# Optimization experiments

Measured on AMD Instinct MI355X. Metric: run time of the kernel, lower is better.

The kernel has to match this reference:

```python
import jax, jax.numpy as jnp
import numpy as np

N, D, M = 4096, 2048, 1000
NL = 2048
MAX_ITER = 5


def setup_inputs() -> dict:
    key = jax.random.key(0)
    k1, k2, k3 = jax.random.split(key, 3)
    fc7 = jax.random.normal(k1, (N, D), dtype=jnp.float32)
    # prior probs: softmax over random logits (row-stochastic, like CNN softmax output)
    probs = jax.nn.softmax(jax.random.normal(k2, (N, M), dtype=jnp.float32), axis=-1)
    labs = jax.random.randint(k3, (NL,), 0, M)
    L = jnp.arange(NL)
    U = jnp.arange(NL, N)
    return {"fc7": fc7, "probs": probs, "labs": labs, "L": L, "U": U}


def _get_W_correlation(fc7):
    # Pearson correlation between rows, negatives clipped to zero (set_negative='hard')
    x = fc7 - fc7.mean(axis=1, keepdims=True)
    norms = jnp.linalg.norm(x, axis=1)  # [n]
    W = (x @ x.T) / jnp.outer(norms, norms)  # [n, n]
    return jax.nn.relu(W)


def _init_probs_prior(probs, labs, L, U):
    n, m = probs.shape
    ps = jnp.zeros((n, m), dtype=probs.dtype)
    ps = ps.at[U].set(probs[U])       # unlabeled: CNN prior
    ps = ps.at[L, labs].set(1.0)      # labeled: one-hot
    return ps


def _replicator(W, ps, max_iter):
    def step(p, _):
        q = p * (W @ p)                              # [n, m]
        q = q / jnp.sum(q, axis=1, keepdims=True)
        return q, None
    ps, _ = jax.lax.scan(step, ps, None, length=max_iter)
    return ps


def reference(fc7, probs, labs, L, U):
    W = _get_W_correlation(fc7)
    ps = _init_probs_prior(probs, labs, L, U)
    ps = _replicator(W, ps, MAX_ITER)
    return ps, W
```

## Files before the change

kernel.cpp:

```cpp
#include <hip/hip_runtime.h>
#include <stdint.h>

#define NS 4096
#define DD 2048
#define MC 1000
#define MP 1024
#define NLAB 2048
#define NU 2048

typedef __attribute__((ext_vector_type(8))) short bf16x8;
typedef __attribute__((ext_vector_type(4))) float f32x4;

__device__ inline unsigned short f2bf(float f) {
  union { float f; uint32_t u; } v; v.f = f;
  uint32_t u = v.u;
  u = u + 0x7fffu + ((u >> 16) & 1u);
  return (unsigned short)(u >> 16);
}
__device__ inline float bf2f(unsigned short h) {
  union { uint32_t u; float f; } v; v.u = ((uint32_t)h) << 16;
  return v.f;
}

__device__ inline void gload_lds16(const void* g, void* l) {
  __builtin_amdgcn_global_load_lds(
      (const __attribute__((address_space(1))) void*)g,
      (__attribute__((address_space(3))) void*)l, 16, 0, 0);
}

__device__ inline float block_sum(float v, float* sm, int tid) {
  #pragma unroll
  for (int o = 32; o > 0; o >>= 1) v += __shfl_down(v, o, 64);
  __syncthreads();
  if ((tid & 63) == 0) sm[tid >> 6] = v;
  __syncthreads();
  return sm[0] + sm[1] + sm[2] + sm[3];
}

__global__ void center_norm_k(const float* __restrict__ fc7,
                              unsigned short* __restrict__ Xc,
                              float* __restrict__ invn) {
  __shared__ float sm[4];
  const int row = blockIdx.x;
  const int tid = threadIdx.x;
  const float4* src = (const float4*)(fc7 + (size_t)row * DD);
  float4 a = src[tid * 2];
  float4 b = src[tid * 2 + 1];
  float s = a.x + a.y + a.z + a.w + b.x + b.y + b.z + b.w;
  s = block_sum(s, sm, tid);
  const float mean = s * (1.f / (float)DD);
  float v0 = a.x - mean, v1 = a.y - mean, v2 = a.z - mean, v3 = a.w - mean;
  float v4 = b.x - mean, v5 = b.y - mean, v6 = b.z - mean, v7 = b.w - mean;
  float ss = v0*v0 + v1*v1 + v2*v2 + v3*v3 + v4*v4 + v5*v5 + v6*v6 + v7*v7;
  ss = block_sum(ss, sm, tid);
  if (tid == 0) invn[row] = rsqrtf(ss);
  ushort4 o0 = make_ushort4(f2bf(v0), f2bf(v1), f2bf(v2), f2bf(v3));
  ushort4 o1 = make_ushort4(f2bf(v4), f2bf(v5), f2bf(v6), f2bf(v7));
  ushort4* dst = (ushort4*)(Xc + (size_t)row * DD);
  dst[tid * 2] = o0;
  dst[tid * 2 + 1] = o1;
}

__global__ void gemm_w_sym(const unsigned short* __restrict__ A,
                           const float* __restrict__ invn,
                           float* __restrict__ outF,
                           unsigned short* __restrict__ outBF) {
  __shared__ __align__(16) unsigned short As[64 * 64];
  __shared__ __align__(16) unsigned short Bs[128 * 64];
  const int tid = threadIdx.x;
  const int wv = tid >> 6;
  const int ln = tid & 63;
  const int wr = wv >> 1, wc = wv & 1;

  int b = (blockIdx.x & 7) * 132 + (blockIdx.x >> 3);
  int r = 0;
  while (b >= 32 - (r >> 1)) { b -= 32 - (r >> 1); ++r; }
  const int c = (r >> 1) + b;
  const int rowBase = r * 64;
  const int colBase = c * 128;
  const bool mirror = (c > (r >> 1));
  const bool bfStraight = (colBase >= NLAB);
  const bool bfMirror = mirror && (rowBase >= NLAB);
  const int fr = ln & 15, kg = ln >> 4;

  f32x4 acc[2][4];
  f32x4 zz = {0.f, 0.f, 0.f, 0.f};
  #pragma unroll
  for (int i = 0; i < 2; ++i)
    #pragma unroll
    for (int j = 0; j < 4; ++j) acc[i][j] = zz;

  const int lrow = ln >> 3;
  const int lcol = ((ln & 7) ^ lrow) * 8;
  const unsigned short* Ap = A + (size_t)(rowBase + lrow) * DD + lcol;
  const unsigned short* Bp = A + (size_t)(colBase + lrow) * DD + lcol;

  for (int k0 = 0; k0 < DD; k0 += 64) {
    if (k0) __syncthreads();
    #pragma unroll
    for (int u = 0; u < 2; ++u) {
      const int rr = wv * 16 + u * 8;
      gload_lds16(Ap + (size_t)rr * DD + k0, &As[rr * 64]);
    }
    #pragma unroll
    for (int u = 0; u < 4; ++u) {
      const int rr = wv * 32 + u * 8;
      gload_lds16(Bp + (size_t)rr * DD + k0, &Bs[rr * 64]);
    }
    __syncthreads();
    #pragma unroll
    for (int kk = 0; kk < 2; ++kk) {
      bf16x8 af[2], bfr[4];
      #pragma unroll
      for (int i = 0; i < 2; ++i) {
        const int rr = wr * 32 + i * 16 + fr;
        af[i] = *(const bf16x8*)&As[rr * 64 + ((kk * 4 + kg) ^ (rr & 7)) * 8];
      }
      #pragma unroll
      for (int j = 0; j < 4; ++j) {
        const int rr = wc * 64 + j * 16 + fr;
        bfr[j] = *(const bf16x8*)&Bs[rr * 64 + ((kk * 4 + kg) ^ (rr & 7)) * 8];
      }
      #pragma unroll
      for (int i = 0; i < 2; ++i)
        #pragma unroll
        for (int j = 0; j < 4; ++j)
          acc[i][j] = __builtin_amdgcn_mfma_f32_16x16x32_bf16(af[i], bfr[j], acc[i][j], 0, 0, 0);
    }
  }

  const int cr = (ln >> 4) * 4;
  const int cc = ln & 15;
  #pragma unroll
  for (int i = 0; i < 2; ++i) {
    const int rb = rowBase + wr * 32 + i * 16 + cr;
    #pragma unroll
    for (int j = 0; j < 4; ++j) {
      const int cb = colBase + wc * 64 + j * 16 + cc;
      const float ic = invn[cb];
      float v[4];
      #pragma unroll
      for (int u = 0; u < 4; ++u) {
        float x = acc[i][j][u] * invn[rb + u] * ic;
        v[u] = x > 0.f ? x : 0.f;
        const size_t o = (size_t)(rb + u) * NS + cb;
        outF[o] = v[u];
        if (bfStraight) outBF[o] = f2bf(v[u]);
      }
      if (mirror) {
        const size_t o = (size_t)cb * NS + rb;
        *(float4*)&outF[o] = make_float4(v[0], v[1], v[2], v[3]);
        if (bfMirror)
          *(ushort4*)&outBF[o] = make_ushort4(f2bf(v[0]), f2bf(v[1]), f2bf(v[2]), f2bf(v[3]));
      }
    }
  }
}

__global__ void gemm_rep(const unsigned short* __restrict__ pT,
                         const unsigned short* __restrict__ Wbf,
                         unsigned short* __restrict__ q0, unsigned short* __restrict__ q1,
                         unsigned short* __restrict__ q2, unsigned short* __restrict__ q3,
                         int kBase) {
  __shared__ __align__(16) unsigned short As[64 * 64];
  __shared__ __align__(16) unsigned short Bs[128 * 64];
  const int tid = threadIdx.x;
  const int wv = tid >> 6;
  const int ln = tid & 63;
  const int wr = wv >> 1, wc = wv & 1;
  const int rowBase = blockIdx.y * 64;
  const int colBase = blockIdx.x * 128;
  const int kOff = kBase + blockIdx.z * 512;
  unsigned short* __restrict__ outF = (blockIdx.z == 0) ? q0 : (blockIdx.z == 1) ? q1
                                    : (blockIdx.z == 2) ? q2 : q3;
  const int fr = ln & 15, kg = ln >> 4;

  f32x4 acc[2][4];
  f32x4 zz = {0.f, 0.f, 0.f, 0.f};
  #pragma unroll
  for (int i = 0; i < 2; ++i)
    #pragma unroll
    for (int j = 0; j < 4; ++j) acc[i][j] = zz;

  const int lrow = ln >> 3;
  const int lcol = ((ln & 7) ^ lrow) * 8;
  const unsigned short* Ap = pT + (size_t)(rowBase + lrow) * NS + kOff + lcol;
  const unsigned short* Bp = Wbf + (size_t)(NLAB + colBase + lrow) * NS + kOff + lcol;

  for (int k0 = 0; k0 < 512; k0 += 64) {
    if (k0) __syncthreads();
    #pragma unroll
    for (int u = 0; u < 2; ++u) {
      const int rr = wv * 16 + u * 8;
      gload_lds16(Ap + (size_t)rr * NS + k0, &As[rr * 64]);
    }
    #pragma unroll
    for (int u = 0; u < 4; ++u) {
      const int rr = wv * 32 + u * 8;
      gload_lds16(Bp + (size_t)rr * NS + k0, &Bs[rr * 64]);
    }
    __syncthreads();
    #pragma unroll
    for (int kk = 0; kk < 2; ++kk) {
      bf16x8 af[2], bfr[4];
      #pragma unroll
      for (int i = 0; i < 2; ++i) {
        const int rr = wr * 32 + i * 16 + fr;
        af[i] = *(const bf16x8*)&As[rr * 64 + ((kk * 4 + kg) ^ (rr & 7)) * 8];
      }
      #pragma unroll
      for (int j = 0; j < 4; ++j) {
        const int rr = wc * 64 + j * 16 + fr;
        bfr[j] = *(const bf16x8*)&Bs[rr * 64 + ((kk * 4 + kg) ^ (rr & 7)) * 8];
      }
      #pragma unroll
      for (int i = 0; i < 2; ++i)
        #pragma unroll
        for (int j = 0; j < 4; ++j)
          acc[i][j] = __builtin_amdgcn_mfma_f32_16x16x32_bf16(af[i], bfr[j], acc[i][j], 0, 0, 0);
    }
  }

  const int cr = (ln >> 4) * 4;
  const int cc = ln & 15;
  #pragma unroll
  for (int i = 0; i < 2; ++i) {
    const int rb = rowBase + wr * 32 + i * 16 + cr;
    #pragma unroll
    for (int j = 0; j < 4; ++j) {
      const int cb = colBase + wc * 64 + j * 16 + cc;
      #pragma unroll
      for (int u = 0; u < 4; ++u)
        outF[(size_t)(rb + u) * NU + cb] = f2bf(acc[i][j][u]);
    }
  }
}

__global__ void wl_gather_k(const int* __restrict__ labs,
                            const unsigned short* __restrict__ Wbf,
                            float* __restrict__ WL) {
  __shared__ unsigned long long masks[32];
  const int m = blockIdx.x;
  const int t = threadIdx.x;
  const int wv = t >> 6, ln = t & 63;
  #pragma unroll
  for (int u = 0; u < 8; ++u) {
    const int w2 = wv * 8 + u;
    unsigned long long msk = __ballot(labs[w2 * 64 + ln] == m);
    if (ln == 0) masks[w2] = msk;
  }
  __syncthreads();
  float acc[8] = {0.f, 0.f, 0.f, 0.f, 0.f, 0.f, 0.f, 0.f};
  for (int w2 = 0; w2 < 32; ++w2) {
    unsigned long long m64 = masks[w2];
    while (m64) {
      const int bit = __ffsll(m64) - 1;
      m64 &= (m64 - 1);
      const int j = w2 * 64 + bit;
      bf16x8 w = *(const bf16x8*)&Wbf[(size_t)j * NS + NLAB + t * 8];
      #pragma unroll
      for (int k = 0; k < 8; ++k) acc[k] += bf2f((unsigned short)w[k]);
    }
  }
  float* dst = WL + (size_t)m * NU + t * 8;
  *(float4*)dst = make_float4(acc[0], acc[1], acc[2], acc[3]);
  *(float4*)(dst + 4) = make_float4(acc[4], acc[5], acc[6], acc[7]);
}

__global__ void init_pT_k(const float* __restrict__ probs, const int* __restrict__ labs,
                          unsigned short* __restrict__ pT) {
  __shared__ float t[32][33];
  const int tx = threadIdx.x, ty = threadIdx.y;
  const int i0 = blockIdx.x * 32, m0 = blockIdx.y * 32;
  const int i = i0 + ty;
  const int m = m0 + tx;
  float v = 0.f;
  if (i < NLAB) v = (m == labs[i]) ? 1.f : 0.f;
  else if (m < MC) v = probs[(size_t)i * MC + m];
  t[ty][tx] = v;
  __syncthreads();
  pT[(size_t)(m0 + ty) * NS + i0 + tx] = f2bf(t[tx][ty]);
}

__global__ void onehot_k(const int* __restrict__ labs, float* __restrict__ ps) {
  const int i = blockIdx.x;
  const int m4 = threadIdx.x * 4;
  if (m4 >= MC) return;
  const int lab = labs[i];
  float4 v;
  v.x = (lab == m4)     ? 1.f : 0.f;
  v.y = (lab == m4 + 1) ? 1.f : 0.f;
  v.z = (lab == m4 + 2) ? 1.f : 0.f;
  v.w = (lab == m4 + 3) ? 1.f : 0.f;
  *(float4*)&ps[(size_t)i * MC + m4] = v;
}

__global__ void colsum_part_k(const unsigned short* __restrict__ q0,
                              const unsigned short* __restrict__ q1,
                              const unsigned short* __restrict__ q2,
                              const unsigned short* __restrict__ q3,
                              const float* __restrict__ WL,
                              const unsigned short* __restrict__ pT,
                              float* __restrict__ pq,
                              float* __restrict__ part) {
  const int i = blockIdx.x * 256 + threadIdx.x;
  const int c = blockIdx.y;
  float s = 0.f;
  #pragma unroll 4
  for (int mm = 0; mm < 64; ++mm) {
    const int m = c * 64 + mm;
    const size_t o = (size_t)m * NU + i;
    const float q = bf2f(q0[o]) + bf2f(q1[o]) + bf2f(q2[o]) + bf2f(q3[o]) + WL[o];
    const float f = bf2f(pT[(size_t)m * NS + NLAB + i]) * q;
    s += f;
    pq[o] = f;
  }
  part[c * NU + i] = s;
}

__global__ void colsum_fin_k(const float* __restrict__ part, float* __restrict__ rsum) {
  const int i = blockIdx.x * 256 + threadIdx.x;
  float s = 0.f;
  #pragma unroll
  for (int c = 0; c < 16; ++c) s += part[c * NU + i];
  rsum[i] = 1.0f / s;
}

__global__ void scale_k(const float* __restrict__ pq,
                        const float* __restrict__ rsum,
                        unsigned short* __restrict__ pT) {
  const int g = blockIdx.x * 256 + threadIdx.x;
  const int idx = g * 4;
  const int i = idx & (NU - 1);
  const int m = idx >> 11;
  float4 p = *(const float4*)(pq + idx);
  float4 r = *(const float4*)(rsum + i);
  ushort4 o = make_ushort4(f2bf(p.x * r.x), f2bf(p.y * r.y),
                           f2bf(p.z * r.z), f2bf(p.w * r.w));
  *(ushort4*)(pT + (size_t)m * NS + NLAB + i) = o;
}

__global__ void final_k(const float* __restrict__ pq,
                        const float* __restrict__ rsum,
                        float* __restrict__ ps) {
  __shared__ float t[32][33];
  const int tx = threadIdx.x, ty = threadIdx.y;
  const int i0 = blockIdx.x * 32, m0 = blockIdx.y * 32;
  t[ty][tx] = pq[(size_t)(m0 + ty) * NU + i0 + tx];
  __syncthreads();
  const int i = i0 + ty, m = m0 + tx;
  if (m < MC)
    ps[(size_t)(NLAB + i) * MC + m] = t[tx][ty] * rsum[i];
}

extern "C" void kernel_launch(void* const* d_in, const int* in_sizes, int n_in,
                              void* d_out, int out_size, void* d_ws, size_t ws_size,
                              hipStream_t stream) {
  const float* fc7   = (const float*)d_in[0];
  const float* probs = (const float*)d_in[1];
  const int*   labs  = (const int*)d_in[2];

  char* ws = (char*)d_ws;
  unsigned short* Xc   = (unsigned short*)(ws);
  unsigned short* Wbf  = (unsigned short*)(ws + (16ull << 20));
  unsigned short* pT   = (unsigned short*)(ws + (48ull << 20));
  unsigned short* q0   = (unsigned short*)(ws + (56ull << 20));
  unsigned short* q1   = (unsigned short*)(ws + (60ull << 20));
  unsigned short* q2   = (unsigned short*)(ws + (64ull << 20));
  unsigned short* q3   = (unsigned short*)(ws + (68ull << 20));
  float*          WL   = (float*)(ws + (72ull << 20));
  float*          pq   = (float*)(ws + (80ull << 20));
  float*          invn = (float*)(ws + (88ull << 20));
  float*          rsum = (float*)(ws + (88ull << 20) + (16ull << 10));
  float*          part = (float*)(ws + (89ull << 20));

  float* out_ps = (float*)d_out;
  float* out_W  = out_ps + (size_t)NS * MC;

  center_norm_k<<<NS, 256, 0, stream>>>(fc7, Xc, invn);

  gemm_w_sym<<<1056, 256, 0, stream>>>(Xc, invn, out_W, Wbf);

  init_pT_k<<<dim3(NS / 32, MP / 32), dim3(32, 32), 0, stream>>>(probs, labs, pT);
  onehot_k<<<NLAB, 256, 0, stream>>>(labs, out_ps);

  wl_gather_k<<<MP, 256, 0, stream>>>(labs, Wbf, WL);

  for (int it = 0; it < 5; ++it) {
    gemm_rep<<<dim3(NU / 128, MP / 64, 4), 256, 0, stream>>>(pT, Wbf, q0, q1, q2, q3, NLAB);
    colsum_part_k<<<dim3(NU / 256, 16), 256, 0, stream>>>(q0, q1, q2, q3, WL, pT, pq, part);
    colsum_fin_k<<<NU / 256, 256, 0, stream>>>(part, rsum);
    if (it < 4)
      scale_k<<<(MP * NU / 4) / 256, 256, 0, stream>>>(pq, rsum, pT);
    else
      final_k<<<dim3(NU / 32, MP / 32), dim3(32, 32), 0, stream>>>(pq, rsum, out_ps);
  }
}
```

Baseline: 252.3 us.

## Double-buffer W GEMM LDS loads and compact pT to unlabeled columns

The symmetric correlation GEMM now uses two LDS buffers, so the global-to-LDS loads for the next K step are issued before the current step's MFMAs, with explicit vmcnt waits and barriers. This is meant to hide load latency behind compute. Separately, the transposed probability matrix pT now stores only the unlabeled columns (stride NU instead of NS), shrinking init, scale and colsum traffic. The cost is doubled LDS per block, which may lower occupancy, and a hand-tuned waitcnt that must match the number of issued loads.

```diff
diff --git a/kernel.cpp b/kernel.cpp
--- a/kernel.cpp
+++ b/kernel.cpp
@@ -65,8 +65,8 @@
                            const float* __restrict__ invn,
                            float* __restrict__ outF,
                            unsigned short* __restrict__ outBF) {
-  __shared__ __align__(16) unsigned short As[64 * 64];
-  __shared__ __align__(16) unsigned short Bs[128 * 64];
+  __shared__ __align__(16) unsigned short As[2][64 * 64];
+  __shared__ __align__(16) unsigned short Bs[2][128 * 64];
   const int tid = threadIdx.x;
   const int wv = tid >> 6;
   const int ln = tid & 63;
@@ -95,31 +95,45 @@
   const unsigned short* Ap = A + (size_t)(rowBase + lrow) * DD + lcol;
   const unsigned short* Bp = A + (size_t)(colBase + lrow) * DD + lcol;
 
-  for (int k0 = 0; k0 < DD; k0 += 64) {
-    if (k0) __syncthreads();
+  auto stage = [&](int step, int buf) {
+    const int k0 = step * 64;
     #pragma unroll
     for (int u = 0; u < 2; ++u) {
       const int rr = wv * 16 + u * 8;
-      gload_lds16(Ap + (size_t)rr * DD + k0, &As[rr * 64]);
+      gload_lds16(Ap + (size_t)rr * DD + k0, &As[buf][rr * 64]);
     }
     #pragma unroll
     for (int u = 0; u < 4; ++u) {
       const int rr = wv * 32 + u * 8;
-      gload_lds16(Bp + (size_t)rr * DD + k0, &Bs[rr * 64]);
-    }
-    __syncthreads();
+      gload_lds16(Bp + (size_t)rr * DD + k0, &Bs[buf][rr * 64]);
+    }
+  };
+
+  stage(0, 0);
+  constexpr int NSTEP = DD / 64;
+  for (int step = 0; step < NSTEP; ++step) {
+    const int cur = step & 1;
+    __builtin_amdgcn_s_barrier();
+    if (step + 1 < NSTEP) {
+      stage(step + 1, cur ^ 1);
+      asm volatile("s_waitcnt vmcnt(6)" ::: "memory");
+    } else {
+      asm volatile("s_waitcnt vmcnt(0)" ::: "memory");
+    }
+    __builtin_amdgcn_s_barrier();
+    __builtin_amdgcn_sched_barrier(0);
     #pragma unroll
     for (int kk = 0; kk < 2; ++kk) {
       bf16x8 af[2], bfr[4];
       #pragma unroll
       for (int i = 0; i < 2; ++i) {
         const int rr = wr * 32 + i * 16 + fr;
-        af[i] = *(const bf16x8*)&As[rr * 64 + ((kk * 4 + kg) ^ (rr & 7)) * 8];
+        af[i] = *(const bf16x8*)&As[cur][rr * 64 + ((kk * 4 + kg) ^ (rr & 7)) * 8];
       }
       #pragma unroll
       for (int j = 0; j < 4; ++j) {
         const int rr = wc * 64 + j * 16 + fr;
-        bfr[j] = *(const bf16x8*)&Bs[rr * 64 + ((kk * 4 + kg) ^ (rr & 7)) * 8];
+        bfr[j] = *(const bf16x8*)&Bs[cur][rr * 64 + ((kk * 4 + kg) ^ (rr & 7)) * 8];
       }
       #pragma unroll
       for (int i = 0; i < 2; ++i)
@@ -160,8 +174,7 @@
 __global__ void gemm_rep(const unsigned short* __restrict__ pT,
                          const unsigned short* __restrict__ Wbf,
                          unsigned short* __restrict__ q0, unsigned short* __restrict__ q1,
-                         unsigned short* __restrict__ q2, unsigned short* __restrict__ q3,
-                         int kBase) {
+                         unsigned short* __restrict__ q2, unsigned short* __restrict__ q3) {
   __shared__ __align__(16) unsigned short As[64 * 64];
   __shared__ __align__(16) unsigned short Bs[128 * 64];
   const int tid = threadIdx.x;
@@ -170,7 +183,7 @@
   const int wr = wv >> 1, wc = wv & 1;
   const int rowBase = blockIdx.y * 64;
   const int colBase = blockIdx.x * 128;
-  const int kOff = kBase + blockIdx.z * 512;
+  const int kRel = blockIdx.z * 512;
   unsigned short* __restrict__ outF = (blockIdx.z == 0) ? q0 : (blockIdx.z == 1) ? q1
                                     : (blockIdx.z == 2) ? q2 : q3;
   const int fr = ln & 15, kg = ln >> 4;
@@ -184,15 +197,15 @@
 
   const int lrow = ln >> 3;
   const int lcol = ((ln & 7) ^ lrow) * 8;
-  const unsigned short* Ap = pT + (size_t)(rowBase + lrow) * NS + kOff + lcol;
-  const unsigned short* Bp = Wbf + (size_t)(NLAB + colBase + lrow) * NS + kOff + lcol;
+  const unsigned short* Ap = pT + (size_t)(rowBase + lrow) * NU + kRel + lcol;
+  const unsigned short* Bp = Wbf + (size_t)(NLAB + colBase + lrow) * NS + NLAB + kRel + lcol;
 
   for (int k0 = 0; k0 < 512; k0 += 64) {
     if (k0) __syncthreads();
     #pragma unroll
     for (int u = 0; u < 2; ++u) {
       const int rr = wv * 16 + u * 8;
-      gload_lds16(Ap + (size_t)rr * NS + k0, &As[rr * 64]);
+      gload_lds16(Ap + (size_t)rr * NU + k0, &As[rr * 64]);
     }
     #pragma unroll
     for (int u = 0; u < 4; ++u) {
@@ -267,19 +280,16 @@
   *(float4*)(dst + 4) = make_float4(acc[4], acc[5], acc[6], acc[7]);
 }
 
-__global__ void init_pT_k(const float* __restrict__ probs, const int* __restrict__ labs,
+__global__ void init_pT_k(const float* __restrict__ probs,
                           unsigned short* __restrict__ pT) {
   __shared__ float t[32][33];
   const int tx = threadIdx.x, ty = threadIdx.y;
   const int i0 = blockIdx.x * 32, m0 = blockIdx.y * 32;
   const int i = i0 + ty;
   const int m = m0 + tx;
-  float v = 0.f;
-  if (i < NLAB) v = (m == labs[i]) ? 1.f : 0.f;
-  else if (m < MC) v = probs[(size_t)i * MC + m];
-  t[ty][tx] = v;
+  t[ty][tx] = (m < MC) ? probs[(size_t)(NLAB + i) * MC + m] : 0.f;
   __syncthreads();
-  pT[(size_t)(m0 + ty) * NS + i0 + tx] = f2bf(t[tx][ty]);
+  pT[(size_t)(m0 + ty) * NU + i0 + tx] = f2bf(t[tx][ty]);
 }
 
 __global__ void onehot_k(const int* __restrict__ labs, float* __restrict__ ps) {
@@ -311,7 +321,7 @@
     const int m = c * 64 + mm;
     const size_t o = (size_t)m * NU + i;
     const float q = bf2f(q0[o]) + bf2f(q1[o]) + bf2f(q2[o]) + bf2f(q3[o]) + WL[o];
-    const float f = bf2f(pT[(size_t)m * NS + NLAB + i]) * q;
+    const float f = bf2f(pT[o]) * q;
     s += f;
     pq[o] = f;
   }
@@ -332,12 +342,11 @@
   const int g = blockIdx.x * 256 + threadIdx.x;
   const int idx = g * 4;
   const int i = idx & (NU - 1);
-  const int m = idx >> 11;
   float4 p = *(const float4*)(pq + idx);
   float4 r = *(const float4*)(rsum + i);
   ushort4 o = make_ushort4(f2bf(p.x * r.x), f2bf(p.y * r.y),
                            f2bf(p.z * r.z), f2bf(p.w * r.w));
-  *(ushort4*)(pT + (size_t)m * NS + NLAB + i) = o;
+  *(ushort4*)(pT + idx) = o;
 }
 
 __global__ void final_k(const float* __restrict__ pq,
@@ -381,13 +390,13 @@
 
   gemm_w_sym<<<1056, 256, 0, stream>>>(Xc, invn, out_W, Wbf);
 
-  init_pT_k<<<dim3(NS / 32, MP / 32), dim3(32, 32), 0, stream>>>(probs, labs, pT);
+  init_pT_k<<<dim3(NU / 32, MP / 32), dim3(32, 32), 0, stream>>>(probs, pT);
   onehot_k<<<NLAB, 256, 0, stream>>>(labs, out_ps);
 
   wl_gather_k<<<MP, 256, 0, stream>>>(labs, Wbf, WL);
 
   for (int it = 0; it < 5; ++it) {
-    gemm_rep<<<dim3(NU / 128, MP / 64, 4), 256, 0, stream>>>(pT, Wbf, q0, q1, q2, q3, NLAB);
+    gemm_rep<<<dim3(NU / 128, MP / 64, 4), 256, 0, stream>>>(pT, Wbf, q0, q1, q2, q3);
     colsum_part_k<<<dim3(NU / 256, 16), 256, 0, stream>>>(q0, q1, q2, q3, WL, pT, pq, part);
     colsum_fin_k<<<NU / 256, 256, 0, stream>>>(part, rsum);
     if (it < 4)
```

New measurement: 254.3 us. Within noise of the previous version (+0.8%).
